# Optimization experiments

Hardware: AMD Instinct MI355X
Metric: run time of the kernel (lower is better)

## Reference

```python
import jax, jax.numpy as jnp
import numpy as np

EPS = 1e-8
INL_TH = 2.0          # RANSAC inl_th default; oneway_transfer_error squared=True
MIN_SAMPLE = 4        # minimal_sample_size for homography
MAX_LO_ITERS = 5      # RANSAC max_lo_iters
DLT_ITERS = 5         # find_homography_dlt_iterated n_iter default
SOFT_INL_TH = 3.0     # find_homography_dlt_iterated soft_inl_th default


def normalize_points(pts):
    # pts: (B,N,2) -> normalized points + (B,3,3) transforms (kornia normalize_points)
    mean = pts.mean(axis=1, keepdims=True)                      # (B,1,2)
    scale = jnp.linalg.norm(pts - mean, axis=-1).mean(axis=-1)  # (B,)
    scale = jnp.asarray(np.sqrt(2.0), pts.dtype) / (scale + EPS)
    pts_n = (pts - mean) * scale[:, None, None]
    mx, my = mean[:, 0, 0], mean[:, 0, 1]
    z = jnp.zeros_like(scale)
    o = jnp.ones_like(scale)
    T = jnp.stack([scale, z, -scale * mx,
                   z, scale, -scale * my,
                   z, z, o], axis=-1).reshape(-1, 3, 3)
    return pts_n, T


def find_homography_dlt(p1, p2, w):
    # weighted normalized DLT: p1,p2 (B,N,2), w (B,N) -> H (B,3,3)
    B = p1.shape[0]
    p1n, T1 = normalize_points(p1)
    p2n, T2 = normalize_points(p2)
    x1, y1 = p1n[..., 0], p1n[..., 1]
    x2, y2 = p2n[..., 0], p2n[..., 1]
    o = jnp.ones_like(x1)
    z = jnp.zeros_like(x1)
    ax = jnp.stack([z, z, z, -x1, -y1, -o, y2 * x1, y2 * y1, y2], axis=-1)  # (B,N,9)
    ay = jnp.stack([x1, y1, o, z, z, z, -x2 * x1, -x2 * y1, -x2], axis=-1)  # (B,N,9)
    A = jnp.stack([ax, ay], axis=2).reshape(B, -1, 9)   # (B,2N,9), ax/ay rows interleaved
    w2 = jnp.repeat(w, 2, axis=1)                       # repeat_interleave to match rows
    AtA = jnp.einsum('bni,bn,bnj->bij', A, w2, A)       # (B,9,9)
    _, _, Vh = jnp.linalg.svd(AtA)
    H = Vh[:, -1].reshape(-1, 3, 3)                     # null vector
    H = jnp.linalg.inv(T2) @ H @ T1                     # denormalize
    return H / (H[:, 2:3, 2:3] + EPS)


def transfer_errors(H, p1, p2, squared=True):
    # oneway_transfer_error: H (B,3,3), p1,p2 (N,2) -> (B,N)
    p1h = jnp.concatenate([p1, jnp.ones_like(p1[..., :1])], axis=-1)  # (N,3)
    proj = jnp.einsum('bij,nj->bni', H, p1h)                          # (B,N,3)
    zc = proj[..., 2:3]
    s = jnp.where(jnp.abs(zc) > EPS, 1.0 / zc, jnp.ones_like(zc))
    pt = proj[..., :2] * s
    err = ((pt - p2) ** 2).sum(-1)
    return err if squared else jnp.sqrt(jnp.maximum(err, 0.0))


def sample_is_valid_for_homography(p1, p2):
    # orientation-consistency of 4-point minimal samples: (B,4,2) -> (B,)
    trip = jnp.array([[0, 1, 2], [0, 2, 3], [0, 1, 3], [1, 2, 3]])
    p1h = jnp.concatenate([p1, jnp.ones_like(p1[..., :1])], axis=-1)
    p2h = jnp.concatenate([p2, jnp.ones_like(p2[..., :1])], axis=-1)
    d1 = jnp.linalg.det(p1h[:, trip])  # (B,4) triple-product signs
    d2 = jnp.linalg.det(p2h[:, trip])
    return jnp.all(jnp.sign(d1) == jnp.sign(d2), axis=1)


def polish_model(kp1, kp2, inl_mask):
    # find_homography_dlt_iterated; inlier subset expressed as zero/one weights
    w = inl_mask.astype(kp1.dtype)[None]  # (1,N)
    p1, p2 = kp1[None], kp2[None]
    H = find_homography_dlt(p1, p2, w)
    for _ in range(DLT_ITERS - 1):
        err = transfer_errors(H, kp1, kp2, squared=False)
        w_new = jnp.exp(-err / (2.0 * SOFT_INL_TH ** 2))
        H = find_homography_dlt(p1, p2, w * w_new)
    return H


def ransac_forward(kp1, kp2, idxs):
    dtype = kp1.dtype
    N = kp1.shape[0]
    kp1s, kp2s = kp1[idxs], kp2[idxs]  # (B,4,2) minimal samples
    valid_sample = sample_is_valid_for_homography(kp1s, kp2s)  # remove_bad_samples (as score mask)
    w = jnp.ones(kp1s.shape[:2], dtype)
    models = find_homography_dlt(kp1s, kp2s, w)                # (B,3,3)
    diag_min = jnp.abs(jnp.diagonal(models, axis1=1, axis2=2)).min(axis=1)
    valid_model = diag_min > 1e-4                              # remove_bad_models (as score mask)
    errors = transfer_errors(models, kp1, kp2)                 # (B,N) verify
    inl = errors <= INL_TH
    scores = inl.astype(dtype).sum(axis=1)
    scores = jnp.where(valid_sample & valid_model, scores, jnp.asarray(-1.0, dtype))
    best = jnp.argmax(scores)
    model, inliers, score = models[best], inl[best], scores[best]
    accept = score > float(MIN_SAMPLE)  # best_score_total init = minimal_sample_size

    def lo_body(carry, _):
        m, il, sc = carry
        m_lo = polish_model(kp1, kp2, il)           # (1,3,3)
        err_lo = transfer_errors(m_lo, kp1, kp2)[0]
        il_lo = err_lo <= INL_TH
        sc_lo = il_lo.astype(dtype).sum()
        better = sc_lo > sc                         # non-improving step is a fixed point == break
        m = jnp.where(better, m_lo[0], m)
        il = jnp.where(better, il_lo, il)
        sc = jnp.where(better, sc_lo, sc)
        return (m, il, sc), None

    (model, inliers, score), _ = jax.lax.scan(lo_body, (model, inliers, score), None, length=MAX_LO_ITERS)
    best_model = jnp.where(accept, model, jnp.zeros((3, 3), dtype))
    best_inliers = jnp.where(accept, inliers, jnp.zeros((N,), bool))
    return best_model, best_inliers


def setup_inputs():
    key = jax.random.key(0)
    k1, k2, k3, k4, k5 = jax.random.split(key, 5)
    N, B = 10000, 2048
    kp1 = jax.random.uniform(k1, (N, 2), jnp.float32) * 1000.0
    H_gt = jnp.array([[1.02, 0.01, 10.0], [-0.02, 0.98, -5.0], [1e-5, -1e-5, 1.0]], jnp.float32)
    p1h = jnp.concatenate([kp1, jnp.ones((N, 1), jnp.float32)], axis=-1)
    proj = p1h @ H_gt.T
    proj = proj[:, :2] / proj[:, 2:3]
    noise = jax.random.normal(k2, (N, 2), jnp.float32) * 0.5
    outliers = jax.random.uniform(k3, (N, 2), jnp.float32) * 1000.0
    is_out = jax.random.uniform(k4, (N,)) < 0.5
    kp2 = jnp.where(is_out[:, None], outliers, proj + noise)
    # minimal-sample indices without replacement (torch: rand.topk(k=4, dim=1))
    rand = jax.random.uniform(k5, (B, N))
    _, idxs = jax.lax.top_k(rand, 4)
    return {"kp1": kp1, "kp2": kp2, "idxs": idxs}


def reference(kp1, kp2, idxs):
    return ransac_forward(kp1, kp2, idxs)
```

## Files before the change

kernel.cpp:

```cpp
#include <hip/hip_runtime.h>
#include <math.h>


struct Hdr {
  int best_idx;
  float best_score;
  int pad0, pad1;
  double nrm[6];
};

__device__ __host__ constexpr int TRI6(int u, int v) {
  return u * 6 - u * (u - 1) / 2 + (v - u);
}

__device__ __forceinline__ float sq_err9(const float h[9], float x1, float y1,
                                         float x2, float y2) {
  float px = h[0] * x1 + h[1] * y1 + h[2];
  float py = h[3] * x1 + h[4] * y1 + h[5];
  float pz = h[6] * x1 + h[7] * y1 + h[8];
  float s  = (fabsf(pz) > 1e-8f) ? (1.0f / pz) : 1.0f;
  float dx = px * s - x2;
  float dy = py * s - y2;
  return dx * dx + dy * dy;
}

__device__ __forceinline__ double sel9d(const double* a, int k) {
  double d = a[0];
  d = (k == 1) ? a[1] : d;
  d = (k == 2) ? a[2] : d;
  d = (k == 3) ? a[3] : d;
  d = (k == 4) ? a[4] : d;
  d = (k == 5) ? a[5] : d;
  d = (k == 6) ? a[6] : d;
  d = (k == 7) ? a[7] : d;
  d = (k == 8) ? a[8] : d;
  return d;
}
__device__ __forceinline__ double sel4d(const double* a, int k) {
  double d = a[0];
  d = (k == 1) ? a[1] : d;
  d = (k == 2) ? a[2] : d;
  d = (k == 3) ? a[3] : d;
  return d;
}

__device__ __forceinline__ void wave_solve9(double r[9], int lane, double* xs) {
  double dself = sel9d(r, lane);
  double tr = (lane < 9) ? dself : 0.0;
#pragma unroll
  for (int m = 1; m <= 8; m <<= 1) tr += __shfl_xor(tr, m);
  double ridge = tr * 1e-12 + 1e-30;
#pragma unroll
  for (int k = 0; k < 9; k++)
    if (lane == k) r[k] += ridge;

  double u[9];
#pragma unroll
  for (int k = 0; k < 9; k++) u[k] = 0.0;
  double invd = 0.0;

#pragma unroll
  for (int j = 0; j < 9; j++) {
    double dj = __shfl(r[j], j);
    dj = (dj > 1e-280) ? dj : 1e-280;
    double is = rsqrt(dj);
    double s = dj * is;
    double Lij = r[j] * is;
    if (lane == j) { Lij = s; invd = is; }
    r[j] = Lij;
    double c[9];
#pragma unroll
    for (int k = j; k < 9; k++) c[k] = __shfl(r[j], k);
#pragma unroll
    for (int k = j; k < 9; k++)
      if (lane == j) u[k] = c[k];
    if (lane > j) {
#pragma unroll
      for (int k = j + 1; k < 9; k++) r[k] -= Lij * c[k];
    }
  }

  double x = 1.0;
#pragma unroll
  for (int it = 0; it < 2; ++it) {
    double acc = x;
    double y = 0.0;
#pragma unroll
    for (int k = 0; k < 9; k++) {
      double yk = __shfl(acc * invd, k);
      if (lane == k) y = yk;
      if (lane > k) acc -= r[k] * yk;
    }
    acc = y;
#pragma unroll
    for (int k = 8; k >= 0; k--) {
      double xk = __shfl(acc * invd, k);
      if (lane == k) x = xk;
      if (lane < k) acc -= u[k] * xk;
    }
    double m2 = (lane < 9) ? fabs(x) : 0.0;
#pragma unroll
    for (int m = 1; m <= 8; m <<= 1) m2 = fmax(m2, __shfl_xor(m2, m));
    x *= 1.0 / m2;
  }
  *xs = x;
}

__device__ __forceinline__ void denorm9(const double hh[9], double mx1,
                                        double my1, double s1, double mx2,
                                        double my2, double s2, float out[9]) {
  double is2 = 1.0 / s2;
  double g0 = is2 * hh[0] + mx2 * hh[6];
  double g1 = is2 * hh[1] + mx2 * hh[7];
  double g2 = is2 * hh[2] + mx2 * hh[8];
  double g3 = is2 * hh[3] + my2 * hh[6];
  double g4 = is2 * hh[4] + my2 * hh[7];
  double g5 = is2 * hh[5] + my2 * hh[8];
  double g6 = hh[6], g7 = hh[7], g8 = hh[8];
  double a = -s1 * mx1, b = -s1 * my1;
  double H0 = s1 * g0, H1 = s1 * g1, H2 = a * g0 + b * g1 + g2;
  double H3 = s1 * g3, H4 = s1 * g4, H5 = a * g3 + b * g4 + g5;
  double H6 = s1 * g6, H7 = s1 * g7, H8 = a * g6 + b * g7 + g8;
  double inv = 1.0 / (H8 + 1e-8);
  out[0] = (float)(H0 * inv);
  out[1] = (float)(H1 * inv);
  out[2] = (float)(H2 * inv);
  out[3] = (float)(H3 * inv);
  out[4] = (float)(H4 * inv);
  out[5] = (float)(H5 * inv);
  out[6] = (float)(H6 * inv);
  out[7] = (float)(H7 * inv);
  out[8] = (float)(H8 * inv);
}

__global__ __launch_bounds__(64, 2) void k_fit_score(
    const float2* __restrict__ kp1, const float2* __restrict__ kp2,
    const int* __restrict__ idxs, int N, float* __restrict__ models,
    float* __restrict__ scores) {
  __shared__ double sA8[8 * 9];
  __shared__ float sH[9];
  const int b = blockIdx.x;
  const int lane = threadIdx.x;

  double X1[4], Y1[4], X2[4], Y2[4];
#pragma unroll
  for (int k = 0; k < 4; k++) {
    int id = idxs[b * 4 + k];
    float2 a = kp1[id];
    float2 c = kp2[id];
    X1[k] = a.x; Y1[k] = a.y; X2[k] = c.x; Y2[k] = c.y;
  }
  const int t0[4] = {0, 0, 0, 1};
  const int t1[4] = {1, 2, 1, 2};
  const int t2[4] = {2, 3, 3, 3};
  bool vs = true;
#pragma unroll
  for (int q = 0; q < 4; q++) {
    int i0 = t0[q], i1 = t1[q], i2 = t2[q];
    double d1 = (X1[i1] - X1[i0]) * (Y1[i2] - Y1[i0]) -
                (X1[i2] - X1[i0]) * (Y1[i1] - Y1[i0]);
    double d2 = (X2[i1] - X2[i0]) * (Y2[i2] - Y2[i0]) -
                (X2[i2] - X2[i0]) * (Y2[i1] - Y2[i0]);
    int sg1 = (d1 > 0.0) ? 1 : ((d1 < 0.0) ? -1 : 0);
    int sg2 = (d2 > 0.0) ? 1 : ((d2 < 0.0) ? -1 : 0);
    vs = vs && (sg1 == sg2);
  }
  double mx1 = (X1[0] + X1[1] + X1[2] + X1[3]) * 0.25;
  double my1 = (Y1[0] + Y1[1] + Y1[2] + Y1[3]) * 0.25;
  double mx2 = (X2[0] + X2[1] + X2[2] + X2[3]) * 0.25;
  double my2 = (Y2[0] + Y2[1] + Y2[2] + Y2[3]) * 0.25;
  double n1 = 0.0, n2 = 0.0;
#pragma unroll
  for (int k = 0; k < 4; k++) {
    double dx = X1[k] - mx1, dy = Y1[k] - my1;
    n1 += sqrt(dx * dx + dy * dy);
    dx = X2[k] - mx2; dy = Y2[k] - my2;
    n2 += sqrt(dx * dx + dy * dy);
  }
  double s1 = sqrt(2.0) / (n1 * 0.25 + 1e-8);
  double s2 = sqrt(2.0) / (n2 * 0.25 + 1e-8);

  if (lane < 8) {
    int k = lane >> 1;
    double xn1 = (sel4d(X1, k) - mx1) * s1;
    double yn1 = (sel4d(Y1, k) - my1) * s1;
    double xn2 = (sel4d(X2, k) - mx2) * s2;
    double yn2 = (sel4d(Y2, k) - my2) * s2;
    bool odd = (lane & 1) != 0;
    sA8[lane * 9 + 0] = odd ? xn1 : 0.0;
    sA8[lane * 9 + 1] = odd ? yn1 : 0.0;
    sA8[lane * 9 + 2] = odd ? 1.0 : 0.0;
    sA8[lane * 9 + 3] = odd ? 0.0 : -xn1;
    sA8[lane * 9 + 4] = odd ? 0.0 : -yn1;
    sA8[lane * 9 + 5] = odd ? 0.0 : -1.0;
    sA8[lane * 9 + 6] = odd ? -xn2 * xn1 : yn2 * xn1;
    sA8[lane * 9 + 7] = odd ? -xn2 * yn1 : yn2 * yn1;
    sA8[lane * 9 + 8] = odd ? -xn2 : yn2;
  }
  __syncthreads();

  double r[9];
  {
    int i = (lane < 9) ? lane : 0;
    double ai[8];
#pragma unroll
    for (int l = 0; l < 8; l++) ai[l] = sA8[l * 9 + i];
#pragma unroll
    for (int j = 0; j < 9; j++) {
      double s = 0.0;
#pragma unroll
      for (int l = 0; l < 8; l++) s += ai[l] * sA8[l * 9 + j];
      r[j] = s;
    }
  }
  double xs;
  wave_solve9(r, lane, &xs);

  double hh[9];
#pragma unroll
  for (int k = 0; k < 9; k++) hh[k] = __shfl(xs, k);

  bool valid = vs;
  if (lane == 0) {
    float Hf[9];
    denorm9(hh, mx1, my1, s1, mx2, my2, s2, Hf);
    bool vm = fminf(fminf(fabsf(Hf[0]), fabsf(Hf[4])), fabsf(Hf[8])) > 1e-4f;
    valid = vs && vm;
#pragma unroll
    for (int j = 0; j < 9; j++) sH[j] = Hf[j];
  }
  __syncthreads();

  float h[9];
#pragma unroll
  for (int j = 0; j < 9; j++) h[j] = sH[j];
  int cnt = 0;
  for (int i = lane; i < N; i += 64) {
    float2 a = kp1[i];
    float2 c = kp2[i];
    cnt += (sq_err9(h, a.x, a.y, c.x, c.y) <= 2.0f) ? 1 : 0;
  }
#pragma unroll
  for (int off = 32; off; off >>= 1) cnt += __shfl_down(cnt, off);
  if (lane == 0) {
    scores[b] = valid ? (float)cnt : -1.0f;
#pragma unroll
    for (int j = 0; j < 9; j++) models[b * 9 + j] = sH[j];
  }
}

__global__ __launch_bounds__(1024) void k_select(
    const float2* __restrict__ kp1, const float2* __restrict__ kp2, int N,
    int B, const float* __restrict__ scores, Hdr* __restrict__ hdr) {
  const int t = threadIdx.x;
  const int lane = t & 63, wid = t >> 6;
  __shared__ float rs[1024];
  __shared__ int ri[1024];

  float bs = -2.0f;
  int bi = 0x7fffffff;
  for (int i = t; i < B; i += 1024) {
    float s = scores[i];
    if (s > bs || (s == bs && i < bi)) { bs = s; bi = i; }
  }
  rs[t] = bs;
  ri[t] = bi;
  __syncthreads();
  for (int off = 512; off; off >>= 1) {
    if (t < off) {
      float s = rs[t + off];
      int i2 = ri[t + off];
      if (s > rs[t] || (s == rs[t] && i2 < ri[t])) { rs[t] = s; ri[t] = i2; }
    }
    __syncthreads();
  }
  if (t == 0) {
    hdr->best_idx = ri[0];
    hdr->best_score = rs[0];
  }

  __shared__ double red[16][4];
  __shared__ double mb[4];
  double sx1 = 0, sy1 = 0, sx2 = 0, sy2 = 0;
  for (int i = t; i < N; i += 1024) {
    float2 a = kp1[i];
    float2 c = kp2[i];
    sx1 += a.x; sy1 += a.y; sx2 += c.x; sy2 += c.y;
  }
#pragma unroll
  for (int off = 32; off; off >>= 1) {
    sx1 += __shfl_down(sx1, off);
    sy1 += __shfl_down(sy1, off);
    sx2 += __shfl_down(sx2, off);
    sy2 += __shfl_down(sy2, off);
  }
  if (lane == 0) {
    red[wid][0] = sx1; red[wid][1] = sy1; red[wid][2] = sx2; red[wid][3] = sy2;
  }
  __syncthreads();
  if (t == 0) {
    double a = 0, b2 = 0, c = 0, d = 0;
    for (int w2 = 0; w2 < 16; w2++) {
      a += red[w2][0]; b2 += red[w2][1]; c += red[w2][2]; d += red[w2][3];
    }
    mb[0] = a / N; mb[1] = b2 / N; mb[2] = c / N; mb[3] = d / N;
  }
  __syncthreads();
  double mx1 = mb[0], my1 = mb[1], mx2 = mb[2], my2 = mb[3];
  double sn1 = 0, sn2 = 0;
  for (int i = t; i < N; i += 1024) {
    float2 a = kp1[i];
    float2 c = kp2[i];
    double dx = a.x - mx1, dy = a.y - my1;
    sn1 += sqrt(dx * dx + dy * dy);
    dx = c.x - mx2; dy = c.y - my2;
    sn2 += sqrt(dx * dx + dy * dy);
  }
#pragma unroll
  for (int off = 32; off; off >>= 1) {
    sn1 += __shfl_down(sn1, off);
    sn2 += __shfl_down(sn2, off);
  }
  __syncthreads();
  if (lane == 0) { red[wid][0] = sn1; red[wid][1] = sn2; }
  __syncthreads();
  if (t == 0) {
    double a = 0, b2 = 0;
    for (int w2 = 0; w2 < 16; w2++) { a += red[w2][0]; b2 += red[w2][1]; }
    hdr->nrm[0] = mx1;
    hdr->nrm[1] = my1;
    hdr->nrm[2] = sqrt(2.0) / (a / N + 1e-8);
    hdr->nrm[3] = mx2;
    hdr->nrm[4] = my2;
    hdr->nrm[5] = sqrt(2.0) / (b2 / N + 1e-8);
  }
}

#define K3_T 512
#define PPT 20

__global__ __launch_bounds__(512, 2) void k_lo(const float2* __restrict__ kp1,
                                               const float2* __restrict__ kp2,
                                               int N,
                                               const float* __restrict__ models,
                                               const Hdr* __restrict__ hdr,
                                               float* __restrict__ out,
                                               int out_size) {
  const int t = threadIdx.x;
  const int lane = t & 63, wid = t >> 6;
  __shared__ float sP[K3_T * 24];
  __shared__ double sP2[24 * 8];
  __shared__ double sC[24];
  __shared__ float sHcur[9];
  __shared__ float sHpol[9];
  __shared__ float sScLo;
  __shared__ int sCnt[8];
  __shared__ double sPar[6];
  __shared__ float sAccept;

  if (t == 0) {
    int bi = hdr->best_idx;
#pragma unroll
    for (int j = 0; j < 9; j++) sHcur[j] = models[bi * 9 + j];
    sAccept = hdr->best_score;
#pragma unroll
    for (int j = 0; j < 6; j++) sPar[j] = hdr->nrm[j];
  }
  __syncthreads();
  const bool accept = sAccept > 4.0f;
  if (!accept) {
    for (int i = t; i < out_size; i += K3_T) out[i] = 0.0f;
    return;
  }
  const float mx1 = (float)sPar[0], my1 = (float)sPar[1], s1 = (float)sPar[2];
  const float mx2 = (float)sPar[3], my2 = (float)sPar[4], s2 = (float)sPar[5];

  float rx1[PPT], ry1[PPT], rx2[PPT], ry2[PPT];
#pragma unroll
  for (int p = 0; p < PPT; p++) {
    int i = p * K3_T + t;
    if (i < N) {
      float2 a = kp1[i];
      float2 c = kp2[i];
      rx1[p] = a.x; ry1[p] = a.y; rx2[p] = c.x; ry2[p] = c.y;
    } else {
      rx1[p] = 0.0f; ry1[p] = 0.0f; rx2[p] = 0.0f; ry2[p] = 0.0f;
    }
  }

  float hc[9];
#pragma unroll
  for (int j = 0; j < 9; j++) hc[j] = sHcur[j];
  unsigned int il = 0u;
#pragma unroll
  for (int p = 0; p < PPT; p++) {
    int i = p * K3_T + t;
    if (i < N && sq_err9(hc, rx1[p], ry1[p], rx2[p], ry2[p]) <= 2.0f)
      il |= (1u << p);
  }
  float sc = sAccept;

  for (int lo = 0; lo < 5; ++lo) {
    for (int j = 0; j < 5; ++j) {
      float hp[9];
      if (j > 0) {
#pragma unroll
        for (int q = 0; q < 9; q++) hp[q] = sHpol[q];
      }
      float a0[6], aX[6], aY[6], aR[6];
#pragma unroll
      for (int k = 0; k < 6; k++) { a0[k] = 0; aX[k] = 0; aY[k] = 0; aR[k] = 0; }
#pragma unroll
      for (int p = 0; p < PPT; p++) {
        int i = p * K3_T + t;
        float w = (i < N && ((il >> p) & 1u)) ? 1.0f : 0.0f;
        if (j > 0) {
          float e = sq_err9(hp, rx1[p], ry1[p], rx2[p], ry2[p]);
          w *= __expf(-sqrtf(fmaxf(e, 0.0f)) * 0.05555555556f);
        }
        float xn1 = (rx1[p] - mx1) * s1, yn1 = (ry1[p] - my1) * s1;
        float xn2 = (rx2[p] - mx2) * s2, yn2 = (ry2[p] - my2) * s2;
        float xx = xn1 * xn1, xy = xn1 * yn1, yy = yn1 * yn1;
        float wx = w * xn2, wy = w * yn2;
        float wr = w * (xn2 * xn2 + yn2 * yn2);
        a0[0] += w * xx;  a0[1] += w * xy;  a0[2] += w * xn1;
        a0[3] += w * yy;  a0[4] += w * yn1; a0[5] += w;
        aX[0] += wx * xx; aX[1] += wx * xy; aX[2] += wx * xn1;
        aX[3] += wx * yy; aX[4] += wx * yn1; aX[5] += wx;
        aY[0] += wy * xx; aY[1] += wy * xy; aY[2] += wy * xn1;
        aY[3] += wy * yy; aY[4] += wy * yn1; aY[5] += wy;
        aR[0] += wr * xx; aR[1] += wr * xy; aR[2] += wr * xn1;
        aR[3] += wr * yy; aR[4] += wr * yn1; aR[5] += wr;
      }
#pragma unroll
      for (int k = 0; k < 6; k++) {
        sP[t * 24 + k] = a0[k];
        sP[t * 24 + 6 + k] = aX[k];
        sP[t * 24 + 12 + k] = aY[k];
        sP[t * 24 + 18 + k] = aR[k];
      }
      __syncthreads();
      if (t < 192) {
        int col = t % 24, grp = t / 24;
        double s = 0.0;
        int base = grp * 64 * 24 + col;
        for (int i2 = 0; i2 < 64; i2++) s += (double)sP[base + i2 * 24];
        sP2[col * 8 + grp] = s;
      }
      __syncthreads();
      if (t < 24) {
        double s = 0.0;
#pragma unroll
        for (int g = 0; g < 8; g++) s += sP2[t * 8 + g];
        sC[t] = s;
      }
      __syncthreads();
      if (wid == 0) {
        int i = (lane < 9) ? lane : 0;
        int bi = i / 3, pi = i - 3 * bi;
        double r[9];
#pragma unroll
        for (int jj = 0; jj < 9; jj++) {
          int bj = jj / 3, pj = jj - 3 * bj;
          int a2 = (pi < pj) ? pi : pj;
          int b2 = (pi < pj) ? pj : pi;
          int t6 = a2 * 3 - a2 * (a2 - 1) / 2 + (b2 - a2);
          double v;
          if (bi == bj)
            v = (bi == 2) ? sC[18 + t6] : sC[t6];
          else if (bi + bj == 1)
            v = 0.0;
          else if (bi + bj == 2)
            v = -sC[6 + t6];
          else
            v = -sC[12 + t6];
          r[jj] = v;
        }
        double xs;
        wave_solve9(r, lane, &xs);
        double hh[9];
#pragma unroll
        for (int k = 0; k < 9; k++) hh[k] = __shfl(xs, k);
        if (lane == 0) {
          float ho[9];
          denorm9(hh, sPar[0], sPar[1], sPar[2], sPar[3], sPar[4], sPar[5],
                  ho);
#pragma unroll
          for (int q = 0; q < 9; q++) sHpol[q] = ho[q];
        }
      }
      __syncthreads();
    }
    float hl[9];
#pragma unroll
    for (int q = 0; q < 9; q++) hl[q] = sHpol[q];
    unsigned int il_lo = 0u;
    int cnt = 0;
#pragma unroll
    for (int p = 0; p < PPT; p++) {
      int i = p * K3_T + t;
      if (i < N && sq_err9(hl, rx1[p], ry1[p], rx2[p], ry2[p]) <= 2.0f) {
        il_lo |= (1u << p);
        cnt++;
      }
    }
#pragma unroll
    for (int off = 32; off; off >>= 1) cnt += __shfl_down(cnt, off);
    if (lane == 0) sCnt[wid] = cnt;
    __syncthreads();
    if (t == 0) {
      int tot = 0;
#pragma unroll
      for (int w2 = 0; w2 < 8; w2++) tot += sCnt[w2];
      sScLo = (float)tot;
    }
    __syncthreads();
    float sc_lo = sScLo;
    if (sc_lo > sc) {
      il = il_lo;
      sc = sc_lo;
      if (t == 0) {
#pragma unroll
        for (int q = 0; q < 9; q++) sHcur[q] = sHpol[q];
      }
    }
    __syncthreads();
  }

  if (t < 9 && t < out_size) out[t] = sHcur[t];
#pragma unroll
  for (int p = 0; p < PPT; p++) {
    int i = p * K3_T + t;
    if (i < N && (9 + i) < out_size)
      out[9 + i] = ((il >> p) & 1u) ? 1.0f : 0.0f;
  }
  for (int i = 9 + N + t; i < out_size; i += K3_T) out[i] = 0.0f;
}

extern "C" void kernel_launch(void* const* d_in, const int* in_sizes, int n_in,
                              void* d_out, int out_size, void* d_ws,
                              size_t ws_size, hipStream_t stream) {
  (void)n_in;
  (void)ws_size;
  const float2* kp1 = (const float2*)d_in[0];
  const float2* kp2 = (const float2*)d_in[1];
  const int* idxs = (const int*)d_in[2];
  const int N = in_sizes[0] / 2;
  const int B = in_sizes[2] / 4;

  float* models = (float*)d_ws;
  float* scores = models + (size_t)B * 9;
  size_t off = (((size_t)B * 10 * sizeof(float)) + 15) & ~(size_t)15;
  Hdr* hdr = (Hdr*)((char*)d_ws + off);
  float* outf = (float*)d_out;

  k_fit_score<<<B, 64, 0, stream>>>(kp1, kp2, idxs, N, models, scores);
  k_select<<<1, 1024, 0, stream>>>(kp1, kp2, N, B, scores, hdr);
  k_lo<<<1, K3_T, 0, stream>>>(kp1, kp2, N, models, hdr, outf, out_size);
}
```

Measured before the change: 689.9 us.

## Widen LO kernel to 1024 threads and reload points from memory instead of registers

The single-block local-optimization kernel now runs 1024 threads with 10 points each instead of 512 threads with 20. It no longer caches the keypoints in per-thread register arrays; every pass reloads them from global memory (through L1/L2) and skips the moment-accumulation math for non-inlier points via a branch. The aim is to cut register pressure and use more lanes in this latency-bound single-block phase, at the cost of repeated global loads, more divergence, and a larger shared reduction buffer.

```diff
diff --git a/kernel.cpp b/kernel.cpp
--- a/kernel.cpp
+++ b/kernel.cpp
@@ -8,10 +8,6 @@
   int pad0, pad1;
   double nrm[6];
 };
-
-__device__ __host__ constexpr int TRI6(int u, int v) {
-  return u * 6 - u * (u - 1) / 2 + (v - u);
-}
 
 __device__ __forceinline__ float sq_err9(const float h[9], float x1, float y1,
                                          float x2, float y2) {
@@ -336,25 +332,26 @@
   }
 }
 
-#define K3_T 512
-#define PPT 20
-
-__global__ __launch_bounds__(512, 2) void k_lo(const float2* __restrict__ kp1,
-                                               const float2* __restrict__ kp2,
-                                               int N,
-                                               const float* __restrict__ models,
-                                               const Hdr* __restrict__ hdr,
-                                               float* __restrict__ out,
-                                               int out_size) {
+#define K3_T 1024
+#define PPT 10
+#define NGRP 16
+
+__global__ __launch_bounds__(K3_T) void k_lo(const float2* __restrict__ kp1,
+                                             const float2* __restrict__ kp2,
+                                             int N,
+                                             const float* __restrict__ models,
+                                             const Hdr* __restrict__ hdr,
+                                             float* __restrict__ out,
+                                             int out_size) {
   const int t = threadIdx.x;
   const int lane = t & 63, wid = t >> 6;
   __shared__ float sP[K3_T * 24];
-  __shared__ double sP2[24 * 8];
+  __shared__ double sP2[24 * NGRP];
   __shared__ double sC[24];
   __shared__ float sHcur[9];
   __shared__ float sHpol[9];
   __shared__ float sScLo;
-  __shared__ int sCnt[8];
+  __shared__ int sCnt[NGRP];
   __shared__ double sPar[6];
   __shared__ float sAccept;
 
@@ -375,28 +372,18 @@
   const float mx1 = (float)sPar[0], my1 = (float)sPar[1], s1 = (float)sPar[2];
   const float mx2 = (float)sPar[3], my2 = (float)sPar[4], s2 = (float)sPar[5];
 
-  float rx1[PPT], ry1[PPT], rx2[PPT], ry2[PPT];
+  float hc[9];
+#pragma unroll
+  for (int j = 0; j < 9; j++) hc[j] = sHcur[j];
+  unsigned int il = 0u;
 #pragma unroll
   for (int p = 0; p < PPT; p++) {
     int i = p * K3_T + t;
     if (i < N) {
       float2 a = kp1[i];
       float2 c = kp2[i];
-      rx1[p] = a.x; ry1[p] = a.y; rx2[p] = c.x; ry2[p] = c.y;
-    } else {
-      rx1[p] = 0.0f; ry1[p] = 0.0f; rx2[p] = 0.0f; ry2[p] = 0.0f;
-    }
-  }
-
-  float hc[9];
-#pragma unroll
-  for (int j = 0; j < 9; j++) hc[j] = sHcur[j];
-  unsigned int il = 0u;
-#pragma unroll
-  for (int p = 0; p < PPT; p++) {
-    int i = p * K3_T + t;
-    if (i < N && sq_err9(hc, rx1[p], ry1[p], rx2[p], ry2[p]) <= 2.0f)
-      il |= (1u << p);
+      if (sq_err9(hc, a.x, a.y, c.x, c.y) <= 2.0f) il |= (1u << p);
+    }
   }
   float sc = sAccept;
 
@@ -413,24 +400,28 @@
 #pragma unroll
       for (int p = 0; p < PPT; p++) {
         int i = p * K3_T + t;
-        float w = (i < N && ((il >> p) & 1u)) ? 1.0f : 0.0f;
-        if (j > 0) {
-          float e = sq_err9(hp, rx1[p], ry1[p], rx2[p], ry2[p]);
-          w *= __expf(-sqrtf(fmaxf(e, 0.0f)) * 0.05555555556f);
+        if (i < N && ((il >> p) & 1u)) {
+          float2 a = kp1[i];
+          float2 c = kp2[i];
+          float w = 1.0f;
+          if (j > 0) {
+            float e = sq_err9(hp, a.x, a.y, c.x, c.y);
+            w = __expf(-sqrtf(fmaxf(e, 0.0f)) * 0.05555555556f);
+          }
+          float xn1 = (a.x - mx1) * s1, yn1 = (a.y - my1) * s1;
+          float xn2 = (c.x - mx2) * s2, yn2 = (c.y - my2) * s2;
+          float xx = xn1 * xn1, xy = xn1 * yn1, yy = yn1 * yn1;
+          float wx = w * xn2, wy = w * yn2;
+          float wr = w * (xn2 * xn2 + yn2 * yn2);
+          a0[0] += w * xx;  a0[1] += w * xy;  a0[2] += w * xn1;
+          a0[3] += w * yy;  a0[4] += w * yn1; a0[5] += w;
+          aX[0] += wx * xx; aX[1] += wx * xy; aX[2] += wx * xn1;
+          aX[3] += wx * yy; aX[4] += wx * yn1; aX[5] += wx;
+          aY[0] += wy * xx; aY[1] += wy * xy; aY[2] += wy * xn1;
+          aY[3] += wy * yy; aY[4] += wy * yn1; aY[5] += wy;
+          aR[0] += wr * xx; aR[1] += wr * xy; aR[2] += wr * xn1;
+          aR[3] += wr * yy; aR[4] += wr * yn1; aR[5] += wr;
         }
-        float xn1 = (rx1[p] - mx1) * s1, yn1 = (ry1[p] - my1) * s1;
-        float xn2 = (rx2[p] - mx2) * s2, yn2 = (ry2[p] - my2) * s2;
-        float xx = xn1 * xn1, xy = xn1 * yn1, yy = yn1 * yn1;
-        float wx = w * xn2, wy = w * yn2;
-        float wr = w * (xn2 * xn2 + yn2 * yn2);
-        a0[0] += w * xx;  a0[1] += w * xy;  a0[2] += w * xn1;
-        a0[3] += w * yy;  a0[4] += w * yn1; a0[5] += w;
-        aX[0] += wx * xx; aX[1] += wx * xy; aX[2] += wx * xn1;
-        aX[3] += wx * yy; aX[4] += wx * yn1; aX[5] += wx;
-        aY[0] += wy * xx; aY[1] += wy * xy; aY[2] += wy * xn1;
-        aY[3] += wy * yy; aY[4] += wy * yn1; aY[5] += wy;
-        aR[0] += wr * xx; aR[1] += wr * xy; aR[2] += wr * xn1;
-        aR[3] += wr * yy; aR[4] += wr * yn1; aR[5] += wr;
       }
 #pragma unroll
       for (int k = 0; k < 6; k++) {
@@ -440,18 +431,18 @@
         sP[t * 24 + 18 + k] = aR[k];
       }
       __syncthreads();
-      if (t < 192) {
+      if (t < 24 * NGRP) {
         int col = t % 24, grp = t / 24;
         double s = 0.0;
         int base = grp * 64 * 24 + col;
         for (int i2 = 0; i2 < 64; i2++) s += (double)sP[base + i2 * 24];
-        sP2[col * 8 + grp] = s;
+        sP2[col * NGRP + grp] = s;
       }
       __syncthreads();
       if (t < 24) {
         double s = 0.0;
 #pragma unroll
-        for (int g = 0; g < 8; g++) s += sP2[t * 8 + g];
+        for (int g = 0; g < NGRP; g++) s += sP2[t * NGRP + g];
         sC[t] = s;
       }
       __syncthreads();
@@ -499,9 +490,13 @@
 #pragma unroll
     for (int p = 0; p < PPT; p++) {
       int i = p * K3_T + t;
-      if (i < N && sq_err9(hl, rx1[p], ry1[p], rx2[p], ry2[p]) <= 2.0f) {
-        il_lo |= (1u << p);
-        cnt++;
+      if (i < N) {
+        float2 a = kp1[i];
+        float2 c = kp2[i];
+        if (sq_err9(hl, a.x, a.y, c.x, c.y) <= 2.0f) {
+          il_lo |= (1u << p);
+          cnt++;
+        }
       }
     }
 #pragma unroll
@@ -511,7 +506,7 @@
     if (t == 0) {
       int tot = 0;
 #pragma unroll
-      for (int w2 = 0; w2 < 8; w2++) tot += sCnt[w2];
+      for (int w2 = 0; w2 < NGRP; w2++) tot += sCnt[w2];
       sScLo = (float)tot;
     }
     __syncthreads();
```

Result: slower. 818.4 us (+18.6%).
